# Performance work log

Hardware: AMD Instinct MI355X
Metric: run time of the kernel (lower is better)

Reference implementation:

```python
import jax, jax.numpy as jnp
import numpy as np

B, L, D = 32, 512, 128
H, D0, D2 = 8, 32, 32
SIGMA = 1.0
NEG = -10000.0


def setup_inputs() -> dict:
    key = jax.random.key(0)
    k_x, k_m, k1, k2, k3, k_w = jax.random.split(key, 6)
    X = jax.random.normal(k_x, (B, L, D), dtype=jnp.float32)
    # random padding mask; guarantee at least one valid item per row
    mask = jax.random.uniform(k_m, (B, L)) < 0.9
    mask = mask.at[:, 0].set(True)
    # nn.Linear(d, H*d0, bias=False): weight shape [H*d0, d], y = x @ W^T
    W1 = SIGMA * jax.random.normal(k1, (H * D0, D), dtype=jnp.float32)
    W2 = SIGMA * jax.random.normal(k2, (H * D0, D), dtype=jnp.float32)
    W3 = SIGMA * jax.random.normal(k3, (H * D2, D), dtype=jnp.float32)
    w = SIGMA * jax.random.normal(k_w, (H, D2), dtype=jnp.float32)
    return {"X": X, "mask": mask, "W1": W1, "W2": W2, "W3": W3, "w": w}


def reference(X, mask, W1, W2, W3, w):
    b, l, d = X.shape
    h, d2 = w.shape
    d0 = W1.shape[0] // h
    Q = (X @ W1.T).reshape(b, l, h, d0)
    K = (X @ W2.T).reshape(b, l, h, d0)
    V = (X @ W3.T).reshape(b, l, h, d2)
    # scores: [B, H, L, L]
    scores = jnp.einsum('blhd,bmhd->bhlm', Q, K) / jnp.sqrt(jnp.asarray(d0, X.dtype))
    # outer-product symmetric pad mask [B,1,L,L]
    am = (mask[:, None, None, :] & mask[:, None, :, None])
    scores = jnp.where(am, scores, jnp.asarray(NEG, X.dtype))
    attn = jax.nn.softmax(scores, axis=-1)
    out = jnp.einsum('bhlm,bmhd->blhd', attn, V)  # [B,L,H,D2]
    v = jnp.einsum('blhd,hd->bl', out, w) / jnp.sqrt(jnp.asarray(h, X.dtype))
    v = jnp.where(mask, v, jnp.asarray(NEG, X.dtype))
    probs = jax.nn.softmax(v, axis=-1)
    return probs
```

## Files before the change

kernel.cpp:

```cpp
#include <hip/hip_runtime.h>
#include <hip/hip_bf16.h>


typedef __attribute__((ext_vector_type(8))) short bf16x8;
typedef __attribute__((ext_vector_type(4))) float f32x4;
typedef __attribute__((ext_vector_type(8))) unsigned short ushort8;
typedef __attribute__((ext_vector_type(4))) unsigned short ushort4v;

#define NEG (-10000.0f)
#define LOG2E 1.4426950408889634f
#define QSCALE (0.17677669529663687f * LOG2E)

__device__ __forceinline__ unsigned short bf16_rn(float x, float* rep) {
  unsigned u = __float_as_uint(x);
  unsigned r = (u + 0x7FFFu + ((u >> 16) & 1u)) >> 16;
  *rep = __uint_as_float(r << 16);
  return (unsigned short)r;
}

__global__ __launch_bounds__(256) void convert_kernel(
    const float* __restrict__ X, const float* __restrict__ W1,
    const float* __restrict__ W2, const float* __restrict__ W3,
    const float* __restrict__ w,
    unsigned short* __restrict__ X2, unsigned short* __restrict__ Wc) {
  const int bx = blockIdx.x, t = threadIdx.x;
  if (bx < 1056) {
    const float* src;
    unsigned short* dst;
    int row, c;
    if (bx < 1024) {
      const size_t flat = (size_t)bx * 2048 + t * 8;
      row = (int)(flat >> 7); c = (int)(flat & 127);
      src = &X[flat];
      dst = &X2[(size_t)row * 256 + c];
    } else {
      const int flat = (bx - 1024) * 2048 + t * 8;
      row = flat >> 7; c = flat & 127;
      src = (row < 256) ? &W1[(size_t)row * 128 + c]
                        : &W2[(size_t)(row - 256) * 128 + c];
      dst = &Wc[(size_t)row * 256 + c];
    }
    float xv[8];
    *(float4*)&xv[0] = *(const float4*)src;
    *(float4*)&xv[4] = *(const float4*)(src + 4);
    ushort8 hi, lo;
#pragma unroll
    for (int i = 0; i < 8; ++i) {
      float hf, lf;
      hi[i] = bf16_rn(xv[i], &hf);
      lo[i] = bf16_rn(xv[i] - hf, &lf);
    }
    *(ushort8*)dst = hi;
    *(ushort8*)(dst + 128) = lo;
  } else {
    __shared__ float uS[8][128];
    if (t < 128) {
#pragma unroll
      for (int h = 0; h < 8; ++h) {
        float acc = 0.f;
#pragma unroll
        for (int d = 0; d < 32; ++d)
          acc += W3[(h * 32 + d) * 128 + t] * w[h * 32 + d];
        uS[h][t] = acc * 0.3535533905932738f;
      }
    }
    __syncthreads();
    {
      const int r = t >> 5, c = (t & 31) * 4;
      float4 v = *(float4*)&uS[r][c];
      float vv[4] = {v.x, v.y, v.z, v.w};
      ushort4v hi, lo;
#pragma unroll
      for (int i = 0; i < 4; ++i) {
        float hf, lf;
        hi[i] = bf16_rn(vv[i], &hf);
        lo[i] = bf16_rn(vv[i] - hf, &lf);
      }
      *(ushort4v*)&Wc[(size_t)(512 + r) * 256 + c] = hi;
      *(ushort4v*)&Wc[(size_t)(512 + r) * 256 + 128 + c] = lo;
    }
    const ushort8 z = {};
    for (int i = t; i < 1792; i += 256)
      *(ushort8*)&Wc[(size_t)520 * 256 + i * 8] = z;
  }
}

__global__ __launch_bounds__(256) void proj_kernel(
    const unsigned short* __restrict__ X2, const unsigned short* __restrict__ Wc,
    unsigned short* __restrict__ Q2, unsigned short* __restrict__ K2,
    float* __restrict__ Vw) {
  __shared__ unsigned short XS[64][72], WSd[64][72], WSx[64][72];
  const int t = threadIdx.x;
  const int row0 = blockIdx.x * 64, col0 = blockIdx.y * 64;
  const int w = t >> 6, lane = t & 63, g = lane >> 4, r16 = lane & 15;
  const int srow = t >> 2, su = (t & 3) * 16;

  f32x4 acc[4];
#pragma unroll
  for (int n = 0; n < 4; ++n) acc[n] = (f32x4){0.f, 0.f, 0.f, 0.f};

  for (int kc = 0; kc < 256; kc += 64) {
    const int kcx = (kc + 128) & 255;
    if (kc) __syncthreads();
    {
      const size_t xo = (size_t)(row0 + srow) * 256 + kc + su;
      const size_t wd = (size_t)(col0 + srow) * 256 + kc + su;
      const size_t wx = (size_t)(col0 + srow) * 256 + kcx + su;
      ushort8 a = *(const ushort8*)&X2[xo];
      ushort8 b = *(const ushort8*)&X2[xo + 8];
      ushort8 c = *(const ushort8*)&Wc[wd];
      ushort8 d = *(const ushort8*)&Wc[wd + 8];
      ushort8 e = *(const ushort8*)&Wc[wx];
      ushort8 f = *(const ushort8*)&Wc[wx + 8];
      *(ushort8*)&XS[srow][su] = a;
      *(ushort8*)&XS[srow][su + 8] = b;
      *(ushort8*)&WSd[srow][su] = c;
      *(ushort8*)&WSd[srow][su + 8] = d;
      *(ushort8*)&WSx[srow][su] = e;
      *(ushort8*)&WSx[srow][su + 8] = f;
    }
    __syncthreads();
#pragma unroll
    for (int ks = 0; ks < 2; ++ks) {
      bf16x8 ah = *(const bf16x8*)&XS[w * 16 + r16][ks * 32 + g * 8];
#pragma unroll
      for (int n = 0; n < 4; ++n) {
        bf16x8 bd = *(const bf16x8*)&WSd[n * 16 + r16][ks * 32 + g * 8];
        bf16x8 bx = *(const bf16x8*)&WSx[n * 16 + r16][ks * 32 + g * 8];
        acc[n] = __builtin_amdgcn_mfma_f32_16x16x32_bf16(ah, bd, acc[n], 0, 0, 0);
        acc[n] = __builtin_amdgcn_mfma_f32_16x16x32_bf16(ah, bx, acc[n], 0, 0, 0);
      }
    }
  }
#pragma unroll
  for (int n = 0; n < 4; ++n) {
    const int col = col0 + n * 16 + r16;
#pragma unroll
    for (int r = 0; r < 4; ++r) {
      const int row = row0 + w * 16 + g * 4 + r;
      const int b = row >> 9, l = row & 511;
      const float val = acc[n][r];
      if (col < 256) {
        const float sv = val * QSCALE;
        float hf, lf;
        const unsigned short hb = bf16_rn(sv, &hf);
        const unsigned short lb = bf16_rn(sv - hf, &lf);
        const size_t o = ((size_t)(b * 8 + (col >> 5)) * 512 + l) * 64 + (col & 31);
        Q2[o] = hb; Q2[o + 32] = lb;
      } else if (col < 512) {
        const int c2 = col - 256;
        float hf, lf;
        const unsigned short hb = bf16_rn(val, &hf);
        const unsigned short lb = bf16_rn(val - hf, &lf);
        const size_t o = ((size_t)(b * 8 + (c2 >> 5)) * 512 + l) * 64 + (c2 & 31);
        K2[o] = hb; K2[o + 32] = lb;
      } else if (col < 520) {
        Vw[(size_t)(b * 8 + (col - 512)) * 512 + l] = val;
      }
    }
  }
}

__global__ __launch_bounds__(512, 4) void attn_kernel(
    const unsigned short* __restrict__ Q2, const unsigned short* __restrict__ K2,
    const float* __restrict__ Vw, const int* __restrict__ mask,
    float* __restrict__ vws) {
  __shared__ unsigned short KS[512][72];
  __shared__ float VwS[512], biasS[512];
  const int t = threadIdx.x;
  const int w = t >> 6, lane = t & 63, g = lane >> 4, r16 = lane & 15;
  const int qbase = blockIdx.x * 256, h = blockIdx.y, b = blockIdx.z;
  const size_t headoff = (size_t)(b * 8 + h) * 512;

#pragma unroll
  for (int i = 0; i < 8; ++i) {
    const int flat = i * 512 + t, row = flat >> 3, cg = (flat & 7) * 8;
    *(ushort8*)&KS[row][cg] = *(const ushort8*)&K2[(headoff + row) * 64 + cg];
  }
  VwS[t] = Vw[headoff + t];
  biasS[t] = mask[b * 512 + t] ? 0.f : NEG * LOG2E;

  bf16x8 qf[2][2];
#pragma unroll
  for (int qt = 0; qt < 2; ++qt)
#pragma unroll
    for (int ks = 0; ks < 2; ++ks)
      qf[qt][ks] = *(const bf16x8*)
          &Q2[(headoff + qbase + w * 32 + qt * 16 + r16) * 64 + ks * 32 + g * 8];

  __syncthreads();

  float m[2] = {-3e38f, -3e38f}, ls[2] = {0.f, 0.f}, vv[2] = {0.f, 0.f};

  for (int c = 0; c < 8; ++c) {
    bf16x8 a0[4], a1[4];
#pragma unroll
    for (int j = 0; j < 4; ++j) {
      a0[j] = *(const bf16x8*)&KS[c * 64 + j * 16 + r16][g * 8];
      a1[j] = *(const bf16x8*)&KS[c * 64 + j * 16 + r16][32 + g * 8];
    }
    float4 bs4[4], vw4[4];
#pragma unroll
    for (int j = 0; j < 4; ++j) {
      bs4[j] = *(const float4*)&biasS[c * 64 + j * 16 + g * 4];
      vw4[j] = *(const float4*)&VwS[c * 64 + j * 16 + g * 4];
    }
#pragma unroll
    for (int qt = 0; qt < 2; ++qt) {
      f32x4 sc[4];
#pragma unroll
      for (int j = 0; j < 4; ++j) {
        f32x4 z = (f32x4){bs4[j].x, bs4[j].y, bs4[j].z, bs4[j].w};
        z = __builtin_amdgcn_mfma_f32_16x16x32_bf16(a0[j], qf[qt][0], z, 0, 0, 0);
        z = __builtin_amdgcn_mfma_f32_16x16x32_bf16(a0[j], qf[qt][1], z, 0, 0, 0);
        z = __builtin_amdgcn_mfma_f32_16x16x32_bf16(a1[j], qf[qt][0], z, 0, 0, 0);
        sc[j] = z;
      }
      float cm01 = fmaxf(fmaxf(sc[0][0], sc[0][1]), fmaxf(sc[0][2], sc[0][3]));
      float cm23 = fmaxf(fmaxf(sc[1][0], sc[1][1]), fmaxf(sc[1][2], sc[1][3]));
      float cm45 = fmaxf(fmaxf(sc[2][0], sc[2][1]), fmaxf(sc[2][2], sc[2][3]));
      float cm67 = fmaxf(fmaxf(sc[3][0], sc[3][1]), fmaxf(sc[3][2], sc[3][3]));
      const float cmax = fmaxf(fmaxf(cm01, cm23), fmaxf(cm45, cm67));
      const float mnew = fmaxf(m[qt], cmax);
      const float f = __builtin_amdgcn_exp2f(m[qt] - mnew);
      m[qt] = mnew;
      float l = ls[qt] * f, v = vv[qt] * f;
#pragma unroll
      for (int j = 0; j < 4; ++j) {
        const float p0 = __builtin_amdgcn_exp2f(sc[j][0] - mnew);
        const float p1 = __builtin_amdgcn_exp2f(sc[j][1] - mnew);
        const float p2 = __builtin_amdgcn_exp2f(sc[j][2] - mnew);
        const float p3 = __builtin_amdgcn_exp2f(sc[j][3] - mnew);
        l += (p0 + p1) + (p2 + p3);
        v = fmaf(p0, vw4[j].x, v);
        v = fmaf(p1, vw4[j].y, v);
        v = fmaf(p2, vw4[j].z, v);
        v = fmaf(p3, vw4[j].w, v);
      }
      ls[qt] = l; vv[qt] = v;
    }
  }
#pragma unroll
  for (int qt = 0; qt < 2; ++qt) {
#pragma unroll
    for (int off = 16; off <= 32; off <<= 1) {
      const float mo = __shfl_xor(m[qt], off);
      const float lo_ = __shfl_xor(ls[qt], off);
      const float vo = __shfl_xor(vv[qt], off);
      const float m2 = fmaxf(m[qt], mo);
      const float fa = __builtin_amdgcn_exp2f(m[qt] - m2);
      const float fb = __builtin_amdgcn_exp2f(mo - m2);
      ls[qt] = ls[qt] * fa + lo_ * fb;
      vv[qt] = vv[qt] * fa + vo * fb;
      m[qt] = m2;
    }
  }
  if (lane < 16) {
#pragma unroll
    for (int qt = 0; qt < 2; ++qt)
      vws[headoff + qbase + w * 32 + qt * 16 + lane] = vv[qt] / ls[qt];
  }
}

__global__ __launch_bounds__(512) void final_kernel(
    const float* __restrict__ vws, const int* __restrict__ mask,
    float* __restrict__ out) {
  const int b = blockIdx.x, l = threadIdx.x;
  __shared__ float redm[8], reds[8];
  float v = 0.f;
#pragma unroll
  for (int h = 0; h < 8; ++h) v += vws[(size_t)(b * 8 + h) * 512 + l];
  if (mask[b * 512 + l] == 0) v = NEG;
  float mx = v;
#pragma unroll
  for (int off = 32; off >= 1; off >>= 1) mx = fmaxf(mx, __shfl_xor(mx, off));
  if ((l & 63) == 0) redm[l >> 6] = mx;
  __syncthreads();
  float M = redm[0];
#pragma unroll
  for (int i = 1; i < 8; ++i) M = fmaxf(M, redm[i]);
  const float e = __expf(v - M);
  float sm = e;
#pragma unroll
  for (int off = 32; off >= 1; off >>= 1) sm += __shfl_xor(sm, off);
  if ((l & 63) == 0) reds[l >> 6] = sm;
  __syncthreads();
  float S = 0.f;
#pragma unroll
  for (int i = 0; i < 8; ++i) S += reds[i];
  out[b * 512 + l] = e / S;
}

extern "C" void kernel_launch(void* const* d_in, const int* in_sizes, int n_in,
                              void* d_out, int out_size, void* d_ws, size_t ws_size,
                              hipStream_t stream) {
  const float* X  = (const float*)d_in[0];
  const int*  mk  = (const int*)d_in[1];
  const float* W1 = (const float*)d_in[2];
  const float* W2 = (const float*)d_in[3];
  const float* W3 = (const float*)d_in[4];
  const float* w  = (const float*)d_in[5];
  float* out = (float*)d_out;

  char* ws = (char*)d_ws;
  unsigned short* X2 = (unsigned short*)ws;
  unsigned short* Wc = X2 + (size_t)16384 * 256;
  unsigned short* Q2 = Wc + (size_t)576 * 256;
  unsigned short* K2 = Q2 + (size_t)32 * 8 * 512 * 64;
  float* Vw  = (float*)(K2 + (size_t)32 * 8 * 512 * 64);
  float* vws = Vw + (size_t)32 * 8 * 512;

  convert_kernel<<<dim3(1057), dim3(256), 0, stream>>>(X, W1, W2, W3, w, X2, Wc);
  proj_kernel<<<dim3(256, 9), dim3(256), 0, stream>>>(X2, Wc, Q2, K2, Vw);
  attn_kernel<<<dim3(2, 8, 32), dim3(512), 0, stream>>>(Q2, K2, Vw, mk, vws);
  final_kernel<<<dim3(32), dim3(512), 0, stream>>>(vws, mk, out);
}
```

Measured before the change: 63.02 us.

## Use one 1024-thread block per head and overlap second K half load with compute

The attention kernel now launches one 1024-thread block per (batch, head) instead of two 512-thread blocks. Each K/Vw/bias tile is therefore staged into shared memory once per head rather than twice. The first half of K is stored and synchronised before compute starts. The second half is fetched into registers early and written to shared memory after the first four chunks, with a second barrier, to overlap global latency with MFMA work. This halves the block count to 256, which may reduce occupancy and latency hiding on a large GPU. The launch bound (1024,4) may also force register spilling.

```diff
diff --git a/kernel.cpp b/kernel.cpp
--- a/kernel.cpp
+++ b/kernel.cpp
@@ -161,7 +161,7 @@
   }
 }
 
-__global__ __launch_bounds__(512, 4) void attn_kernel(
+__global__ __launch_bounds__(1024, 4) void attn_kernel(
     const unsigned short* __restrict__ Q2, const unsigned short* __restrict__ K2,
     const float* __restrict__ Vw, const int* __restrict__ mask,
     float* __restrict__ vws) {
@@ -169,16 +169,37 @@
   __shared__ float VwS[512], biasS[512];
   const int t = threadIdx.x;
   const int w = t >> 6, lane = t & 63, g = lane >> 4, r16 = lane & 15;
-  const int qbase = blockIdx.x * 256, h = blockIdx.y, b = blockIdx.z;
-  const size_t headoff = (size_t)(b * 8 + h) * 512;
-
-#pragma unroll
-  for (int i = 0; i < 8; ++i) {
-    const int flat = i * 512 + t, row = flat >> 3, cg = (flat & 7) * 8;
-    *(ushort8*)&KS[row][cg] = *(const ushort8*)&K2[(headoff + row) * 64 + cg];
-  }
-  VwS[t] = Vw[headoff + t];
-  biasS[t] = mask[b * 512 + t] ? 0.f : NEG * LOG2E;
+  const int head = blockIdx.x;
+  const int b = head >> 3;
+  const size_t headoff = (size_t)head * 512;
+
+  ushort8 kA0, kA1;
+  {
+    const int f0 = t, f1 = 1024 + t;
+    kA0 = *(const ushort8*)&K2[headoff * 64 + f0 * 8];
+    kA1 = *(const ushort8*)&K2[headoff * 64 + f1 * 8];
+  }
+  float vwA = 0.f, biasA = 0.f;
+  if (t < 256) vwA = Vw[headoff + t];
+  else if (t < 512) biasA = mask[b * 512 + (t - 256)] ? 0.f : NEG * LOG2E;
+
+  {
+    const int f0 = t, f1 = 1024 + t;
+    *(ushort8*)&KS[f0 >> 3][(f0 & 7) * 8] = kA0;
+    *(ushort8*)&KS[f1 >> 3][(f1 & 7) * 8] = kA1;
+  }
+  if (t < 256) VwS[t] = vwA;
+  else if (t < 512) biasS[t - 256] = biasA;
+
+  ushort8 kB0, kB1;
+  {
+    const int f2 = 2048 + t, f3 = 3072 + t;
+    kB0 = *(const ushort8*)&K2[headoff * 64 + f2 * 8];
+    kB1 = *(const ushort8*)&K2[headoff * 64 + f3 * 8];
+  }
+  float vwB = 0.f, biasB = 0.f;
+  if (t < 256) vwB = Vw[headoff + 256 + t];
+  else if (t < 512) biasB = mask[b * 512 + 256 + (t - 256)] ? 0.f : NEG * LOG2E;
 
   bf16x8 qf[2][2];
 #pragma unroll
@@ -186,60 +207,77 @@
 #pragma unroll
     for (int ks = 0; ks < 2; ++ks)
       qf[qt][ks] = *(const bf16x8*)
-          &Q2[(headoff + qbase + w * 32 + qt * 16 + r16) * 64 + ks * 32 + g * 8];
+          &Q2[(headoff + w * 32 + qt * 16 + r16) * 64 + ks * 32 + g * 8];
 
   __syncthreads();
 
   float m[2] = {-3e38f, -3e38f}, ls[2] = {0.f, 0.f}, vv[2] = {0.f, 0.f};
 
-  for (int c = 0; c < 8; ++c) {
-    bf16x8 a0[4], a1[4];
-#pragma unroll
-    for (int j = 0; j < 4; ++j) {
-      a0[j] = *(const bf16x8*)&KS[c * 64 + j * 16 + r16][g * 8];
-      a1[j] = *(const bf16x8*)&KS[c * 64 + j * 16 + r16][32 + g * 8];
-    }
-    float4 bs4[4], vw4[4];
-#pragma unroll
-    for (int j = 0; j < 4; ++j) {
-      bs4[j] = *(const float4*)&biasS[c * 64 + j * 16 + g * 4];
-      vw4[j] = *(const float4*)&VwS[c * 64 + j * 16 + g * 4];
-    }
-#pragma unroll
-    for (int qt = 0; qt < 2; ++qt) {
-      f32x4 sc[4];
-#pragma unroll
-      for (int j = 0; j < 4; ++j) {
-        f32x4 z = (f32x4){bs4[j].x, bs4[j].y, bs4[j].z, bs4[j].w};
-        z = __builtin_amdgcn_mfma_f32_16x16x32_bf16(a0[j], qf[qt][0], z, 0, 0, 0);
-        z = __builtin_amdgcn_mfma_f32_16x16x32_bf16(a0[j], qf[qt][1], z, 0, 0, 0);
-        z = __builtin_amdgcn_mfma_f32_16x16x32_bf16(a1[j], qf[qt][0], z, 0, 0, 0);
-        sc[j] = z;
-      }
-      float cm01 = fmaxf(fmaxf(sc[0][0], sc[0][1]), fmaxf(sc[0][2], sc[0][3]));
-      float cm23 = fmaxf(fmaxf(sc[1][0], sc[1][1]), fmaxf(sc[1][2], sc[1][3]));
-      float cm45 = fmaxf(fmaxf(sc[2][0], sc[2][1]), fmaxf(sc[2][2], sc[2][3]));
-      float cm67 = fmaxf(fmaxf(sc[3][0], sc[3][1]), fmaxf(sc[3][2], sc[3][3]));
-      const float cmax = fmaxf(fmaxf(cm01, cm23), fmaxf(cm45, cm67));
-      const float mnew = fmaxf(m[qt], cmax);
-      const float f = __builtin_amdgcn_exp2f(m[qt] - mnew);
-      m[qt] = mnew;
-      float l = ls[qt] * f, v = vv[qt] * f;
-#pragma unroll
-      for (int j = 0; j < 4; ++j) {
-        const float p0 = __builtin_amdgcn_exp2f(sc[j][0] - mnew);
-        const float p1 = __builtin_amdgcn_exp2f(sc[j][1] - mnew);
-        const float p2 = __builtin_amdgcn_exp2f(sc[j][2] - mnew);
-        const float p3 = __builtin_amdgcn_exp2f(sc[j][3] - mnew);
-        l += (p0 + p1) + (p2 + p3);
-        v = fmaf(p0, vw4[j].x, v);
-        v = fmaf(p1, vw4[j].y, v);
-        v = fmaf(p2, vw4[j].z, v);
-        v = fmaf(p3, vw4[j].w, v);
-      }
-      ls[qt] = l; vv[qt] = v;
-    }
-  }
+#define COMPUTE_CHUNK(c)                                                       \
+  {                                                                            \
+    bf16x8 a0[4], a1[4];                                                       \
+    _Pragma("unroll") for (int j = 0; j < 4; ++j) {                            \
+      a0[j] = *(const bf16x8*)&KS[(c) * 64 + j * 16 + r16][g * 8];             \
+      a1[j] = *(const bf16x8*)&KS[(c) * 64 + j * 16 + r16][32 + g * 8];        \
+    }                                                                          \
+    float4 bs4[4], vw4[4];                                                     \
+    _Pragma("unroll") for (int j = 0; j < 4; ++j) {                            \
+      bs4[j] = *(const float4*)&biasS[(c) * 64 + j * 16 + g * 4];              \
+      vw4[j] = *(const float4*)&VwS[(c) * 64 + j * 16 + g * 4];                \
+    }                                                                          \
+    _Pragma("unroll") for (int qt = 0; qt < 2; ++qt) {                         \
+      f32x4 sc[4];                                                             \
+      _Pragma("unroll") for (int j = 0; j < 4; ++j) {                          \
+        f32x4 z = (f32x4){bs4[j].x, bs4[j].y, bs4[j].z, bs4[j].w};             \
+        z = __builtin_amdgcn_mfma_f32_16x16x32_bf16(a0[j], qf[qt][0], z, 0, 0, 0); \
+        z = __builtin_amdgcn_mfma_f32_16x16x32_bf16(a0[j], qf[qt][1], z, 0, 0, 0); \
+        z = __builtin_amdgcn_mfma_f32_16x16x32_bf16(a1[j], qf[qt][0], z, 0, 0, 0); \
+        sc[j] = z;                                                             \
+      }                                                                        \
+      float cm01 = fmaxf(fmaxf(sc[0][0], sc[0][1]), fmaxf(sc[0][2], sc[0][3])); \
+      float cm23 = fmaxf(fmaxf(sc[1][0], sc[1][1]), fmaxf(sc[1][2], sc[1][3])); \
+      float cm45 = fmaxf(fmaxf(sc[2][0], sc[2][1]), fmaxf(sc[2][2], sc[2][3])); \
+      float cm67 = fmaxf(fmaxf(sc[3][0], sc[3][1]), fmaxf(sc[3][2], sc[3][3])); \
+      const float cmax = fmaxf(fmaxf(cm01, cm23), fmaxf(cm45, cm67));          \
+      const float mnew = fmaxf(m[qt], cmax);                                   \
+      const float fsc = __builtin_amdgcn_exp2f(m[qt] - mnew);                  \
+      m[qt] = mnew;                                                            \
+      float l = ls[qt] * fsc, v = vv[qt] * fsc;                                \
+      _Pragma("unroll") for (int j = 0; j < 4; ++j) {                          \
+        const float p0 = __builtin_amdgcn_exp2f(sc[j][0] - mnew);              \
+        const float p1 = __builtin_amdgcn_exp2f(sc[j][1] - mnew);              \
+        const float p2 = __builtin_amdgcn_exp2f(sc[j][2] - mnew);              \
+        const float p3 = __builtin_amdgcn_exp2f(sc[j][3] - mnew);              \
+        l += (p0 + p1) + (p2 + p3);                                            \
+        v = fmaf(p0, vw4[j].x, v);                                             \
+        v = fmaf(p1, vw4[j].y, v);                                             \
+        v = fmaf(p2, vw4[j].z, v);                                             \
+        v = fmaf(p3, vw4[j].w, v);                                             \
+      }                                                                        \
+      ls[qt] = l; vv[qt] = v;                                                  \
+    }                                                                          \
+  }
+
+  COMPUTE_CHUNK(0)
+  COMPUTE_CHUNK(1)
+  COMPUTE_CHUNK(2)
+  COMPUTE_CHUNK(3)
+
+  {
+    const int f2 = 2048 + t, f3 = 3072 + t;
+    *(ushort8*)&KS[f2 >> 3][(f2 & 7) * 8] = kB0;
+    *(ushort8*)&KS[f3 >> 3][(f3 & 7) * 8] = kB1;
+  }
+  if (t < 256) VwS[256 + t] = vwB;
+  else if (t < 512) biasS[256 + (t - 256)] = biasB;
+  __syncthreads();
+
+  COMPUTE_CHUNK(4)
+  COMPUTE_CHUNK(5)
+  COMPUTE_CHUNK(6)
+  COMPUTE_CHUNK(7)
+#undef COMPUTE_CHUNK
+
 #pragma unroll
   for (int qt = 0; qt < 2; ++qt) {
 #pragma unroll
@@ -258,7 +296,7 @@
   if (lane < 16) {
 #pragma unroll
     for (int qt = 0; qt < 2; ++qt)
-      vws[headoff + qbase + w * 32 + qt * 16 + lane] = vv[qt] / ls[qt];
+      vws[headoff + w * 32 + qt * 16 + lane] = vv[qt] / ls[qt];
   }
 }
 
@@ -312,6 +350,6 @@
 
   convert_kernel<<<dim3(1057), dim3(256), 0, stream>>>(X, W1, W2, W3, w, X2, Wc);
   proj_kernel<<<dim3(256, 9), dim3(256), 0, stream>>>(X2, Wc, Q2, K2, Vw);
-  attn_kernel<<<dim3(2, 8, 32), dim3(512), 0, stream>>>(Q2, K2, Vw, mk, vws);
+  attn_kernel<<<dim3(256), dim3(1024), 0, stream>>>(Q2, K2, Vw, mk, vws);
   final_kernel<<<dim3(32), dim3(512), 0, stream>>>(vws, mk, out);
 }
```

After: 86.40 us. 37.1% more time.
